# Kernel tuning notes

Hardware: AMD Instinct MI355X
Metric: run time of the kernel (lower is better)

## Reference

```python
import jax, jax.numpy as jnp
import numpy as np

B = 512
N_ENT = 100000
N_REL = 64
D = 200          # embed_dim
D1 = 10          # embed_shape (emb_dim1)
D2 = 20          # embed_dim // embed_shape (emb_dim2)
K = 3            # kernel_size
C = 32           # out_channels
FC_IN = C * (2 * D1 - K + 1) * (D2 - K + 1)  # 32*18*18 = 10368
EPS = 1e-5       # BatchNorm eps
LS = 0.1         # label_smoothing
LAM = 1e-5       # kg_l2_loss_lambda


def setup_inputs() -> dict:
    key = jax.random.key(0)
    ks = jax.random.split(key, 8)
    return dict(
        entity_w=jax.random.normal(ks[0], (N_ENT, D), jnp.float32) * 0.1,
        relation_w=jax.random.normal(ks[1], (N_REL, D), jnp.float32) * 0.1,
        conv_w=jax.random.normal(ks[2], (C, 1, K, K), jnp.float32) * 0.1,
        conv_b=jnp.zeros((C,), jnp.float32),
        fc_w=jax.random.normal(ks[3], (D, FC_IN), jnp.float32) * 0.02,
        fc_b=jnp.zeros((D,), jnp.float32),
        b=jnp.zeros((N_ENT,), jnp.float32),
        bn0_g=jnp.ones((1,), jnp.float32), bn0_b=jnp.zeros((1,), jnp.float32),
        bn1_g=jnp.ones((C,), jnp.float32), bn1_b=jnp.zeros((C,), jnp.float32),
        bn2_g=jnp.ones((D,), jnp.float32), bn2_b=jnp.zeros((D,), jnp.float32),
        h=jax.random.randint(ks[4], (B,), 0, N_ENT),
        r=jax.random.randint(ks[5], (B,), 0, N_REL),
        pos_t=jax.random.randint(ks[6], (B,), 0, N_ENT),
    )


def _bn(x, g, b, axes, shape):
    # training-mode batchnorm (batch statistics), biased variance as in torch
    m = jnp.mean(x, axes, keepdims=True)
    v = jnp.var(x, axes, keepdims=True)
    return (x - m) * jax.lax.rsqrt(v + EPS) * g.reshape(shape) + b.reshape(shape)


def _l2_mean(x):
    # torch: mean(sum(x**2, dim=1) / 2)
    return jnp.mean(jnp.sum(x * x, axis=1) / 2.0)


def reference(entity_w, relation_w, conv_w, conv_b, fc_w, fc_b, b,
              bn0_g, bn0_b, bn1_g, bn1_b, bn2_g, bn2_b, h, r, pos_t):
    h_e = entity_w[h].reshape(B, 1, D1, D2)
    r_e = relation_w[r].reshape(B, 1, D1, D2)
    x = jnp.concatenate([h_e, r_e], axis=2)           # [B,1,2*D1,D2]
    x = _bn(x, bn0_g, bn0_b, (0, 2, 3), (1, 1, 1, 1))
    x = jax.lax.conv_general_dilated(
        x, conv_w, (1, 1), 'VALID',
        dimension_numbers=('NCHW', 'OIHW', 'NCHW')) + conv_b.reshape(1, C, 1, 1)
    x = _bn(x, bn1_g, bn1_b, (0, 2, 3), (1, C, 1, 1))
    x = jax.nn.relu(x).reshape(B, -1)                 # [B, FC_IN]
    x = x @ fc_w.T + fc_b                             # [B, D]
    x = _bn(x, bn2_g, bn2_b, (0,), (1, D))
    x = jax.nn.leaky_relu(x)                          # slope 0.01 = torch default
    scores = x @ entity_w.T + b                       # [B, N_ENT]
    # BCEWithLogits with smoothed label y = (1-LS)*onehot(pos_t) + 1/N_ENT,
    # loss = mean(softplus(s) - s*y); one-hot never materialized.
    sp_sum = jnp.sum(jax.nn.softplus(scores))
    xy_sum = jnp.sum(scores) / N_ENT + (1.0 - LS) * jnp.sum(
        scores[jnp.arange(B), pos_t])
    kg_loss = (sp_sum - xy_sum) / (B * N_ENT)
    l2 = _l2_mean(h_e) + _l2_mean(r_e) + _l2_mean(conv_w) + _l2_mean(fc_w)
    return kg_loss + LAM * l2
```

## Files before the change

### kernel.cpp

```cpp
#include <hip/hip_runtime.h>
#include <math.h>

#define NB_B 512
#define NE 100000
#define DD 200
#define CC 32
#define FCIN 10368
#define HW 324
#define BNEPS 1e-5f
#define KP 224
#define NTILE 1563

typedef __attribute__((ext_vector_type(8))) short short8;
typedef __attribute__((ext_vector_type(4))) float floatx4;


static __device__ __forceinline__ float blk_reduce(float v, volatile float* sbuf) {
  for (int o = 32; o > 0; o >>= 1) v += __shfl_down(v, o, 64);
  int lane = threadIdx.x & 63, wid = threadIdx.x >> 6;
  if (lane == 0) sbuf[wid] = v;
  __syncthreads();
  float r = 0.f;
  int nw = (blockDim.x + 63) >> 6;
  if ((int)threadIdx.x < nw) r = sbuf[threadIdx.x];
  if (threadIdx.x < 64) {
    for (int o = 32; o > 0; o >>= 1) r += __shfl_down(r, o, 64);
  }
  __syncthreads();
  return r;
}

static __device__ __forceinline__ unsigned short f32_to_bf16(float f) {
  unsigned int u = __float_as_uint(f);
  u += 0x7fffu + ((u >> 16) & 1u);
  return (unsigned short)(u >> 16);
}
static __device__ __forceinline__ float bf16_to_f32(unsigned short b) {
  return __uint_as_float(((unsigned int)b) << 16);
}

__global__ void k_gather(const float* __restrict__ ent, const float* __restrict__ rel,
                         const int* __restrict__ h, const int* __restrict__ r,
                         float* __restrict__ x0, double* dacc) {
  int b = blockIdx.x;
  int hi = h[b], ri = r[b];
  float s = 0.f, sq = 0.f;
  for (int i = threadIdx.x; i < 400; i += blockDim.x) {
    float v = (i < 200) ? ent[(long)hi * DD + i] : rel[(long)ri * DD + (i - 200)];
    x0[b * 400 + i] = v;
    s += v; sq += v * v;
  }
  __shared__ float sbuf[8];
  float ts = blk_reduce(s, sbuf);
  float tq = blk_reduce(sq, sbuf);
  if (threadIdx.x == 0) {
    atomicAdd(&dacc[0], (double)ts);
    atomicAdd(&dacc[1], (double)tq);
  }
}

__global__ __launch_bounds__(256) void k_cvt(const float* __restrict__ ent,
                                             unsigned short* __restrict__ entb,
                                             const float* __restrict__ fcw,
                                             unsigned short* __restrict__ fcwb,
                                             double* dacc) {
  if (blockIdx.x < 21875) {
    int i4 = blockIdx.x * 256 + threadIdx.x;
    int row = i4 / 56;
    int c4 = (i4 - row * 56) * 4;
    ushort4 o;
    if (c4 < 200) {
      const float4 v = *(const float4*)&ent[(long)row * DD + c4];
      o.x = f32_to_bf16(v.x); o.y = f32_to_bf16(v.y);
      o.z = f32_to_bf16(v.z); o.w = f32_to_bf16(v.w);
    } else {
      o.x = 0; o.y = 0; o.z = 0; o.w = 0;
    }
    *(ushort4*)&entb[(long)row * KP + c4] = o;
  } else {
    int g = (blockIdx.x - 21875) * 256 + threadIdx.x;
    float sq = 0.f;
    if (g < 259200) {
      const float4* s = (const float4*)(fcw + (long)g * 8);
      float4 u = s[0], v = s[1];
      sq = u.x*u.x + u.y*u.y + u.z*u.z + u.w*u.w
         + v.x*v.x + v.y*v.y + v.z*v.z + v.w*v.w;
      ushort4 o0, o1;
      o0.x = f32_to_bf16(u.x); o0.y = f32_to_bf16(u.y);
      o0.z = f32_to_bf16(u.z); o0.w = f32_to_bf16(u.w);
      o1.x = f32_to_bf16(v.x); o1.y = f32_to_bf16(v.y);
      o1.z = f32_to_bf16(v.z); o1.w = f32_to_bf16(v.w);
      ushort4* d = (ushort4*)(fcwb + (long)g * 8);
      d[0] = o0; d[1] = o1;
    }
    __shared__ float sbuf[8];
    float tq = blk_reduce(sq, sbuf);
    if (threadIdx.x == 0) atomicAdd(&dacc[67], (double)tq);
  }
}

__global__ __launch_bounds__(256) void k_conv(const float* __restrict__ x0,
                       const float* __restrict__ convw, const float* __restrict__ convb,
                       const float* __restrict__ g0, const float* __restrict__ b0,
                       unsigned short* __restrict__ yb, double* dacc) {
  __shared__ float xs[400], wsm[288], cbs[32], ssum[32], ssq[32];
  __shared__ float a0s, s0s;
  int b = blockIdx.x, t = threadIdx.x;
  for (int i = t; i < 400; i += 256) xs[i] = x0[b * 400 + i];
  for (int i = t; i < 288; i += 256) wsm[i] = convw[i];
  if (t < 32) cbs[t] = convb[t];
  if (t == 0) {
    double m = dacc[0] / 204800.0;
    double v = dacc[1] / 204800.0 - m * m;
    float a = g0[0] * rsqrtf((float)v + BNEPS);
    a0s = a; s0s = b0[0] - (float)m * a;
  }
  __syncthreads();
  float a0 = a0s, s0 = s0s;
  for (int i = t; i < 400; i += 256) xs[i] = a0 * xs[i] + s0;
  __syncthreads();
  int c = t >> 3, sub = t & 7;
  const float* w = &wsm[c * 9];
  float cb = cbs[c];
  float s = 0.f, sq = 0.f;
  for (int e = sub; e < HW; e += 8) {
    int oh = e / 18, ow = e - oh * 18;
    const float* xp = &xs[oh * 20 + ow];
    float acc = cb
       + xp[0] * w[0] + xp[1] * w[1] + xp[2] * w[2]
       + xp[20] * w[3] + xp[21] * w[4] + xp[22] * w[5]
       + xp[40] * w[6] + xp[41] * w[7] + xp[42] * w[8];
    yb[(long)b * FCIN + c * HW + e] = f32_to_bf16(acc);
    s += acc; sq += acc * acc;
  }
  s += __shfl_xor(s, 1, 64); sq += __shfl_xor(sq, 1, 64);
  s += __shfl_xor(s, 2, 64); sq += __shfl_xor(sq, 2, 64);
  s += __shfl_xor(s, 4, 64); sq += __shfl_xor(sq, 4, 64);
  if (sub == 0) { ssum[c] = s; ssq[c] = sq; }
  __syncthreads();
  if (t < 32) {
    atomicAdd(&dacc[2 + t], (double)ssum[t]);
    atomicAdd(&dacc[34 + t], (double)ssq[t]);
  }
}

__global__ void k_stats1(const float* __restrict__ g1, const float* __restrict__ b1,
                         const float* __restrict__ convw,
                         float* __restrict__ a1, float* __restrict__ sh1, double* dacc) {
  int t = threadIdx.x;
  if (t < 32) {
    double cnt = 512.0 * 324.0;
    double m = dacc[2 + t] / cnt, v = dacc[34 + t] / cnt - m * m;
    float a = g1[t] * rsqrtf((float)v + BNEPS);
    a1[t] = a; sh1[t] = b1[t] - (float)m * a;
  }
  float sq = 0.f;
  for (int i = t; i < 288; i += 64) { float w = convw[i]; sq += w * w; }
  for (int o = 32; o > 0; o >>= 1) sq += __shfl_down(sq, o, 64);
  if (t == 0) dacc[66] = (double)sq;
}

__global__ __launch_bounds__(256) void k_prep(unsigned short* __restrict__ yb,
                                              const float* __restrict__ a1,
                                              const float* __restrict__ sh1) {
  __shared__ float a1s[32], sh1s[32];
  int t = threadIdx.x;
  if (t < 32) { a1s[t] = a1[t]; sh1s[t] = sh1[t]; }
  __syncthreads();
  int g = blockIdx.x * 256 + t;
  int row = g / 1296;
  int c8 = (g - row * 1296) * 8;
  unsigned short* p = yb + (long)row * FCIN + c8;
  ushort4 v0 = ((ushort4*)p)[0], v1 = ((ushort4*)p)[1];
  unsigned short e[8] = {v0.x, v0.y, v0.z, v0.w, v1.x, v1.y, v1.z, v1.w};
#pragma unroll
  for (int j = 0; j < 8; j++) {
    int c = (c8 + j) / HW;
    float f = a1s[c] * bf16_to_f32(e[j]) + sh1s[c];
    e[j] = f32_to_bf16(fmaxf(f, 0.f));
  }
  v0.x = e[0]; v0.y = e[1]; v0.z = e[2]; v0.w = e[3];
  v1.x = e[4]; v1.y = e[5]; v1.z = e[6]; v1.w = e[7];
  ((ushort4*)p)[0] = v0; ((ushort4*)p)[1] = v1;
}

__global__ __launch_bounds__(64) void k_fc_mfma(const unsigned short* __restrict__ yb,
                                                const unsigned short* __restrict__ fcwb,
                                                float* __restrict__ Cfc) {
  int wid = blockIdx.x;
  int ks = wid >> 5, rem = wid & 31;
  int mt = rem >> 2, nt = rem & 3;
  int lane = threadIdx.x;
  int quad = lane >> 4, lr = lane & 15;
  int m0 = mt * 64, n0 = nt * 64;
  int kbeg = ks * 192;

  const unsigned short* arow[4];
  const unsigned short* brow[4];
#pragma unroll
  for (int mi = 0; mi < 4; mi++)
    arow[mi] = yb + (long)(m0 + mi * 16 + lr) * FCIN + quad * 8 + kbeg;
#pragma unroll
  for (int ni = 0; ni < 4; ni++) {
    int d = n0 + ni * 16 + lr;
    if (d > DD - 1) d = DD - 1;
    brow[ni] = fcwb + (long)d * FCIN + quad * 8 + kbeg;
  }

  floatx4 acc[4][4];
#pragma unroll
  for (int i = 0; i < 4; i++)
#pragma unroll
    for (int j = 0; j < 4; j++) acc[i][j] = (floatx4){0.f, 0.f, 0.f, 0.f};

  short8 acur[4], bcur[4], anxt[4], bnxt[4];
#pragma unroll
  for (int mi = 0; mi < 4; mi++) acur[mi] = *(const short8*)(arow[mi]);
#pragma unroll
  for (int ni = 0; ni < 4; ni++) bcur[ni] = *(const short8*)(brow[ni]);

#pragma unroll
  for (int c = 0; c < 6; c++) {
    if (c < 5) {
#pragma unroll
      for (int mi = 0; mi < 4; mi++) anxt[mi] = *(const short8*)(arow[mi] + (c + 1) * 32);
#pragma unroll
      for (int ni = 0; ni < 4; ni++) bnxt[ni] = *(const short8*)(brow[ni] + (c + 1) * 32);
    }
#pragma unroll
    for (int ni = 0; ni < 4; ni++)
#pragma unroll
      for (int mi = 0; mi < 4; mi++)
        acc[mi][ni] = __builtin_amdgcn_mfma_f32_16x16x32_bf16(acur[mi], bcur[ni], acc[mi][ni], 0, 0, 0);
#pragma unroll
    for (int mi = 0; mi < 4; mi++) acur[mi] = anxt[mi];
#pragma unroll
    for (int ni = 0; ni < 4; ni++) bcur[ni] = bnxt[ni];
  }

#pragma unroll
  for (int ni = 0; ni < 4; ni++) {
    int d = n0 + ni * 16 + lr;
    if (d < DD) {
#pragma unroll
      for (int mi = 0; mi < 4; mi++) {
        int mbase = m0 + mi * 16 + quad * 4;
#pragma unroll
        for (int rg = 0; rg < 4; rg++)
          atomicAdd(&Cfc[(mbase + rg) * DD + d], acc[mi][ni][rg]);
      }
    }
  }
}

__global__ void k_bn2stats(const float* __restrict__ Cfc, const float* __restrict__ fcb,
                           const float* __restrict__ g2, const float* __restrict__ b2,
                           float* __restrict__ a2, float* __restrict__ b2c) {
  int d = blockIdx.x, lane = threadIdx.x;
  float s = 0.f, sq = 0.f;
  for (int b = lane; b < NB_B; b += 64) {
    float v = Cfc[b * DD + d] + fcb[d];
    s += v; sq += v * v;
  }
  for (int o = 32; o > 0; o >>= 1) { s += __shfl_down(s, o, 64); sq += __shfl_down(sq, o, 64); }
  if (lane == 0) {
    float m = s / 512.f, v = sq / 512.f - m * m;
    float a = g2[d] * rsqrtf(v + BNEPS);
    a2[d] = a; b2c[d] = b2[d] - m * a;
  }
}

__global__ __launch_bounds__(256) void k_xfinal(const float* __restrict__ Cfc,
                         const float* __restrict__ fcb,
                         const float* __restrict__ a2, const float* __restrict__ b2c,
                         const float* __restrict__ ent, const float* __restrict__ bias,
                         const int* __restrict__ pos,
                         float* __restrict__ xf, unsigned short* __restrict__ xfb,
                         double* dacc) {
  __shared__ float xs[224];
  __shared__ float sbuf[8];
  int b = blockIdx.x, t = threadIdx.x;
  if (t < KP) {
    float xv = 0.f;
    if (t < DD) {
      float v = Cfc[b * DD + t] + fcb[t];
      xv = a2[t] * v + b2c[t];
      xv = xv >= 0.f ? xv : 0.01f * xv;
      xf[b * DD + t] = xv;
    }
    xfb[b * KP + t] = f32_to_bf16(xv);
    xs[t] = xv;
  }
  __syncthreads();
  int e = pos[b];
  float s = (t < DD) ? xs[t] * ent[(long)e * DD + t] : 0.f;
  float ts = blk_reduce(s, sbuf);
  if (t == 0) atomicAdd(&dacc[70], (double)(ts + bias[e]));
}

__global__ __launch_bounds__(512, 2) void k_scores2(
    const unsigned short* __restrict__ entb,
    const unsigned short* __restrict__ xfb,
    const float* __restrict__ bias, double* dacc) {
  __shared__ float sbuf[8];
  int t = threadIdx.x;
  int wv = t >> 6, lane = t & 63;
  int quad = lane >> 4, lr = lane & 15;

  short8 af[4][7];
#pragma unroll
  for (int mi = 0; mi < 4; mi++) {
    const unsigned short* ap = xfb + (size_t)(wv * 64 + mi * 16 + lr) * KP + quad * 8;
#pragma unroll
    for (int kc = 0; kc < 7; kc++) af[mi][kc] = *(const short8*)(ap + kc * 32);
  }

  float sp = 0.f, ss = 0.f;
  for (int tile = blockIdx.x; tile < NTILE; tile += gridDim.x) {
    int e0 = tile * 64;
    const unsigned short* bp[4];
    int eidx[4];
#pragma unroll
    for (int ni = 0; ni < 4; ni++) {
      int e = e0 + ni * 16 + lr;
      eidx[ni] = e;
      if (e > NE - 1) e = NE - 1;
      bp[ni] = entb + (size_t)e * KP + quad * 8;
    }
    floatx4 acc[4][4];
#pragma unroll
    for (int i = 0; i < 4; i++)
#pragma unroll
      for (int j = 0; j < 4; j++) acc[i][j] = (floatx4){0.f, 0.f, 0.f, 0.f};

    short8 bcur[4], bnxt[4];
#pragma unroll
    for (int ni = 0; ni < 4; ni++) bcur[ni] = *(const short8*)(bp[ni]);
#pragma unroll
    for (int kc = 0; kc < 7; kc++) {
      if (kc < 6) {
#pragma unroll
        for (int ni = 0; ni < 4; ni++) bnxt[ni] = *(const short8*)(bp[ni] + (kc + 1) * 32);
      }
#pragma unroll
      for (int ni = 0; ni < 4; ni++)
#pragma unroll
        for (int mi = 0; mi < 4; mi++)
          acc[mi][ni] = __builtin_amdgcn_mfma_f32_16x16x32_bf16(af[mi][kc], bcur[ni], acc[mi][ni], 0, 0, 0);
#pragma unroll
      for (int ni = 0; ni < 4; ni++) bcur[ni] = bnxt[ni];
    }
#pragma unroll
    for (int ni = 0; ni < 4; ni++) {
      if (eidx[ni] < NE) {
        float be = bias[eidx[ni]];
#pragma unroll
        for (int mi = 0; mi < 4; mi++) {
#pragma unroll
          for (int rg = 0; rg < 4; rg++) {
            float s = acc[mi][ni][rg] + be;
            sp += fmaxf(s, 0.f) + __logf(1.f + __expf(-fabsf(s)));
            ss += s;
          }
        }
      }
    }
  }
  float tsp = blk_reduce(sp, sbuf);
  float tss = blk_reduce(ss, sbuf);
  if (t == 0) {
    atomicAdd(&dacc[68], (double)tsp);
    atomicAdd(&dacc[69], (double)tss);
  }
}

__global__ void k_final(const double* dacc, float* out) {
  double SP = dacc[68], S2 = dacc[69], S3 = dacc[70];
  double xy = S2 / (double)NE + 0.9 * S3;
  double kg = (SP - xy) / ((double)NB_B * (double)NE);
  double l2 = dacc[1] / 204800.0 + dacc[66] / 576.0 + dacc[67] / 400.0;
  out[0] = (float)(kg + 1e-5 * l2);
}

extern "C" void kernel_launch(void* const* d_in, const int* in_sizes, int n_in,
                              void* d_out, int out_size, void* d_ws, size_t ws_size,
                              hipStream_t stream) {
  const float* ent   = (const float*)d_in[0];
  const float* rel   = (const float*)d_in[1];
  const float* convw = (const float*)d_in[2];
  const float* convb = (const float*)d_in[3];
  const float* fcw   = (const float*)d_in[4];
  const float* fcb   = (const float*)d_in[5];
  const float* bias  = (const float*)d_in[6];
  const float* g0    = (const float*)d_in[7];
  const float* b0    = (const float*)d_in[8];
  const float* g1    = (const float*)d_in[9];
  const float* b1    = (const float*)d_in[10];
  const float* g2    = (const float*)d_in[11];
  const float* b2    = (const float*)d_in[12];
  const int*   h     = (const int*)d_in[13];
  const int*   r     = (const int*)d_in[14];
  const int*   pos   = (const int*)d_in[15];

  char* ws = (char*)d_ws;
  double* dacc = (double*)(ws + 0);
  float* a1  = (float*)(ws + 16384);
  float* sh1 = (float*)(ws + 16384 + 128);
  float* a2  = (float*)(ws + 16384 + 256);
  float* b2c = (float*)(ws + 16384 + 1056);
  float* x0  = (float*)(ws + 32768);
  float* Cfc = (float*)(ws + 851968);
  float* xf  = (float*)(ws + 1261568);
  unsigned short* yb   = (unsigned short*)(ws + 1671168);
  unsigned short* fcwb = (unsigned short*)(ws + 12288000);
  unsigned short* xfb  = (unsigned short*)(ws + 16435200);
  unsigned short* entb = (unsigned short*)(ws + 16664576);

  hipMemsetAsync(dacc, 0, 8192, stream);
  hipMemsetAsync(Cfc, 0, 409600, stream);

  k_cvt<<<22888, 256, 0, stream>>>(ent, entb, fcw, fcwb, dacc);
  k_gather<<<512, 256, 0, stream>>>(ent, rel, h, r, x0, dacc);
  k_conv<<<512, 256, 0, stream>>>(x0, convw, convb, g0, b0, yb, dacc);
  k_stats1<<<1, 64, 0, stream>>>(g1, b1, convw, a1, sh1, dacc);
  k_prep<<<2592, 256, 0, stream>>>(yb, a1, sh1);
  k_fc_mfma<<<1728, 64, 0, stream>>>(yb, fcwb, Cfc);
  k_bn2stats<<<200, 64, 0, stream>>>(Cfc, fcb, g2, b2, a2, b2c);
  k_xfinal<<<512, 256, 0, stream>>>(Cfc, fcb, a2, b2c, ent, bias, pos, xf, xfb, dacc);
  k_scores2<<<256, 512, 0, stream>>>(entb, xfb, bias, dacc);
  k_final<<<1, 1, 0, stream>>>(dacc, (float*)d_out);
}
```

Baseline: 328.9 us.

## Fuse gather into convert, drop stats kernel, rework FC and scores grids

Folds the gather into the bf16 convert kernel and widens its per-thread work to 8 elements. The BN1 stats computation moves into k_prep and the conv-weight L2 into k_final, which removes a launch. The FC GEMM becomes 32 blocks of 4 waves that split K and reduce through shared memory, replacing atomics and the Cfc memset. The scores kernel is regridded to 391x4 blocks of 256 threads, each wave handling 32 rows, with double-buffered B loads. Together this cuts launches and atomic traffic, but the FC stage now runs on only 32 blocks, which risks low GPU occupancy.

```diff
diff --git a/kernel.cpp b/kernel.cpp
--- a/kernel.cpp
+++ b/kernel.cpp
@@ -11,6 +11,10 @@
 #define KP 224
 #define NTILE 1563
 
+#define ENT_BLKS 10938
+#define FCW_BLKS 1013
+#define GATH_OFF (ENT_BLKS + FCW_BLKS)
+
 typedef __attribute__((ext_vector_type(8))) short short8;
 typedef __attribute__((ext_vector_type(4))) float floatx4;
 
@@ -39,46 +43,37 @@
   return __uint_as_float(((unsigned int)b) << 16);
 }
 
-__global__ void k_gather(const float* __restrict__ ent, const float* __restrict__ rel,
-                         const int* __restrict__ h, const int* __restrict__ r,
-                         float* __restrict__ x0, double* dacc) {
-  int b = blockIdx.x;
-  int hi = h[b], ri = r[b];
-  float s = 0.f, sq = 0.f;
-  for (int i = threadIdx.x; i < 400; i += blockDim.x) {
-    float v = (i < 200) ? ent[(long)hi * DD + i] : rel[(long)ri * DD + (i - 200)];
-    x0[b * 400 + i] = v;
-    s += v; sq += v * v;
-  }
-  __shared__ float sbuf[8];
-  float ts = blk_reduce(s, sbuf);
-  float tq = blk_reduce(sq, sbuf);
-  if (threadIdx.x == 0) {
-    atomicAdd(&dacc[0], (double)ts);
-    atomicAdd(&dacc[1], (double)tq);
-  }
-}
-
 __global__ __launch_bounds__(256) void k_cvt(const float* __restrict__ ent,
                                              unsigned short* __restrict__ entb,
                                              const float* __restrict__ fcw,
                                              unsigned short* __restrict__ fcwb,
+                                             const float* __restrict__ rel,
+                                             const int* __restrict__ h,
+                                             const int* __restrict__ r,
+                                             float* __restrict__ x0,
                                              double* dacc) {
-  if (blockIdx.x < 21875) {
-    int i4 = blockIdx.x * 256 + threadIdx.x;
-    int row = i4 / 56;
-    int c4 = (i4 - row * 56) * 4;
-    ushort4 o;
-    if (c4 < 200) {
-      const float4 v = *(const float4*)&ent[(long)row * DD + c4];
-      o.x = f32_to_bf16(v.x); o.y = f32_to_bf16(v.y);
-      o.z = f32_to_bf16(v.z); o.w = f32_to_bf16(v.w);
-    } else {
-      o.x = 0; o.y = 0; o.z = 0; o.w = 0;
-    }
-    *(ushort4*)&entb[(long)row * KP + c4] = o;
-  } else {
-    int g = (blockIdx.x - 21875) * 256 + threadIdx.x;
+  if (blockIdx.x < ENT_BLKS) {
+    int g = blockIdx.x * 256 + threadIdx.x;
+    if (g < 2800000) {
+      int row = g / 28;
+      int c8 = (g - row * 28) * 8;
+      ushort4 o0, o1;
+      if (c8 < 200) {
+        const float4* s = (const float4*)(ent + (long)row * DD + c8);
+        float4 u = s[0], v = s[1];
+        o0.x = f32_to_bf16(u.x); o0.y = f32_to_bf16(u.y);
+        o0.z = f32_to_bf16(u.z); o0.w = f32_to_bf16(u.w);
+        o1.x = f32_to_bf16(v.x); o1.y = f32_to_bf16(v.y);
+        o1.z = f32_to_bf16(v.z); o1.w = f32_to_bf16(v.w);
+      } else {
+        o0.x = o0.y = o0.z = o0.w = 0;
+        o1.x = o1.y = o1.z = o1.w = 0;
+      }
+      ushort4* d = (ushort4*)(entb + (long)row * KP + c8);
+      d[0] = o0; d[1] = o1;
+    }
+  } else if (blockIdx.x < GATH_OFF) {
+    int g = (blockIdx.x - ENT_BLKS) * 256 + threadIdx.x;
     float sq = 0.f;
     if (g < 259200) {
       const float4* s = (const float4*)(fcw + (long)g * 8);
@@ -96,6 +91,22 @@
     __shared__ float sbuf[8];
     float tq = blk_reduce(sq, sbuf);
     if (threadIdx.x == 0) atomicAdd(&dacc[67], (double)tq);
+  } else {
+    int b = blockIdx.x - GATH_OFF;
+    int hi = h[b], ri = r[b];
+    float s = 0.f, sq = 0.f;
+    for (int i = threadIdx.x; i < 400; i += 256) {
+      float v = (i < 200) ? ent[(long)hi * DD + i] : rel[(long)ri * DD + (i - 200)];
+      x0[b * 400 + i] = v;
+      s += v; sq += v * v;
+    }
+    __shared__ float sbuf[8];
+    float ts = blk_reduce(s, sbuf);
+    float tq = blk_reduce(sq, sbuf);
+    if (threadIdx.x == 0) {
+      atomicAdd(&dacc[0], (double)ts);
+      atomicAdd(&dacc[1], (double)tq);
+    }
   }
 }
 
@@ -144,28 +155,18 @@
   }
 }
 
-__global__ void k_stats1(const float* __restrict__ g1, const float* __restrict__ b1,
-                         const float* __restrict__ convw,
-                         float* __restrict__ a1, float* __restrict__ sh1, double* dacc) {
+__global__ __launch_bounds__(256) void k_prep(unsigned short* __restrict__ yb,
+                                              const float* __restrict__ g1,
+                                              const float* __restrict__ b1,
+                                              const double* __restrict__ dacc) {
+  __shared__ float a1s[32], sh1s[32];
   int t = threadIdx.x;
   if (t < 32) {
     double cnt = 512.0 * 324.0;
     double m = dacc[2 + t] / cnt, v = dacc[34 + t] / cnt - m * m;
     float a = g1[t] * rsqrtf((float)v + BNEPS);
-    a1[t] = a; sh1[t] = b1[t] - (float)m * a;
-  }
-  float sq = 0.f;
-  for (int i = t; i < 288; i += 64) { float w = convw[i]; sq += w * w; }
-  for (int o = 32; o > 0; o >>= 1) sq += __shfl_down(sq, o, 64);
-  if (t == 0) dacc[66] = (double)sq;
-}
-
-__global__ __launch_bounds__(256) void k_prep(unsigned short* __restrict__ yb,
-                                              const float* __restrict__ a1,
-                                              const float* __restrict__ sh1) {
-  __shared__ float a1s[32], sh1s[32];
-  int t = threadIdx.x;
-  if (t < 32) { a1s[t] = a1[t]; sh1s[t] = sh1[t]; }
+    a1s[t] = a; sh1s[t] = b1[t] - (float)m * a;
+  }
   __syncthreads();
   int g = blockIdx.x * 256 + t;
   int row = g / 1296;
@@ -184,27 +185,27 @@
   ((ushort4*)p)[0] = v0; ((ushort4*)p)[1] = v1;
 }
 
-__global__ __launch_bounds__(64) void k_fc_mfma(const unsigned short* __restrict__ yb,
+__global__ __launch_bounds__(256, 2) void k_fc2(const unsigned short* __restrict__ yb,
                                                 const unsigned short* __restrict__ fcwb,
                                                 float* __restrict__ Cfc) {
-  int wid = blockIdx.x;
-  int ks = wid >> 5, rem = wid & 31;
-  int mt = rem >> 2, nt = rem & 3;
-  int lane = threadIdx.x;
+  __shared__ float red[4][64][64];
+  int bid = blockIdx.x;
+  int mt = bid >> 2, nt = bid & 3;
+  int m0 = mt * 64, n0 = nt * 64;
+  int t = threadIdx.x, wv = t >> 6, lane = t & 63;
   int quad = lane >> 4, lr = lane & 15;
-  int m0 = mt * 64, n0 = nt * 64;
-  int kbeg = ks * 192;
+  long kbeg = (long)wv * 2592;
 
   const unsigned short* arow[4];
   const unsigned short* brow[4];
 #pragma unroll
   for (int mi = 0; mi < 4; mi++)
-    arow[mi] = yb + (long)(m0 + mi * 16 + lr) * FCIN + quad * 8 + kbeg;
+    arow[mi] = yb + (long)(m0 + mi * 16 + lr) * FCIN + kbeg + quad * 8;
 #pragma unroll
   for (int ni = 0; ni < 4; ni++) {
     int d = n0 + ni * 16 + lr;
     if (d > DD - 1) d = DD - 1;
-    brow[ni] = fcwb + (long)d * FCIN + quad * 8 + kbeg;
+    brow[ni] = fcwb + (long)d * FCIN + kbeg + quad * 8;
   }
 
   floatx4 acc[4][4];
@@ -213,42 +214,48 @@
 #pragma unroll
     for (int j = 0; j < 4; j++) acc[i][j] = (floatx4){0.f, 0.f, 0.f, 0.f};
 
-  short8 acur[4], bcur[4], anxt[4], bnxt[4];
-#pragma unroll
-  for (int mi = 0; mi < 4; mi++) acur[mi] = *(const short8*)(arow[mi]);
-#pragma unroll
-  for (int ni = 0; ni < 4; ni++) bcur[ni] = *(const short8*)(brow[ni]);
-
-#pragma unroll
-  for (int c = 0; c < 6; c++) {
-    if (c < 5) {
-#pragma unroll
-      for (int mi = 0; mi < 4; mi++) anxt[mi] = *(const short8*)(arow[mi] + (c + 1) * 32);
-#pragma unroll
-      for (int ni = 0; ni < 4; ni++) bnxt[ni] = *(const short8*)(brow[ni] + (c + 1) * 32);
-    }
+  short8 sA[3][4], sB[3][4];
+#pragma unroll
+  for (int c = 0; c < 3; c++) {
+#pragma unroll
+    for (int mi = 0; mi < 4; mi++) sA[c][mi] = *(const short8*)(arow[mi] + c * 32);
+#pragma unroll
+    for (int ni = 0; ni < 4; ni++) sB[c][ni] = *(const short8*)(brow[ni] + c * 32);
+  }
+  for (int c3 = 0; c3 < 27; c3++) {
+    int cc = c3 * 3;
+#pragma unroll
+    for (int j = 0; j < 3; j++) {
+#pragma unroll
+      for (int ni = 0; ni < 4; ni++)
+#pragma unroll
+        for (int mi = 0; mi < 4; mi++)
+          acc[mi][ni] = __builtin_amdgcn_mfma_f32_16x16x32_bf16(sA[j][mi], sB[j][ni], acc[mi][ni], 0, 0, 0);
+      int nxt = cc + j + 3;
+      if (nxt < 81) {
+#pragma unroll
+        for (int mi = 0; mi < 4; mi++) sA[j][mi] = *(const short8*)(arow[mi] + nxt * 32);
+#pragma unroll
+        for (int ni = 0; ni < 4; ni++) sB[j][ni] = *(const short8*)(brow[ni] + nxt * 32);
+      }
+    }
+  }
+
+#pragma unroll
+  for (int mi = 0; mi < 4; mi++)
 #pragma unroll
     for (int ni = 0; ni < 4; ni++)
 #pragma unroll
-      for (int mi = 0; mi < 4; mi++)
-        acc[mi][ni] = __builtin_amdgcn_mfma_f32_16x16x32_bf16(acur[mi], bcur[ni], acc[mi][ni], 0, 0, 0);
-#pragma unroll
-    for (int mi = 0; mi < 4; mi++) acur[mi] = anxt[mi];
-#pragma unroll
-    for (int ni = 0; ni < 4; ni++) bcur[ni] = bnxt[ni];
-  }
-
-#pragma unroll
-  for (int ni = 0; ni < 4; ni++) {
-    int d = n0 + ni * 16 + lr;
-    if (d < DD) {
-#pragma unroll
-      for (int mi = 0; mi < 4; mi++) {
-        int mbase = m0 + mi * 16 + quad * 4;
-#pragma unroll
-        for (int rg = 0; rg < 4; rg++)
-          atomicAdd(&Cfc[(mbase + rg) * DD + d], acc[mi][ni][rg]);
-      }
+      for (int rg = 0; rg < 4; rg++)
+        red[wv][mi * 16 + quad * 4 + rg][ni * 16 + lr] = acc[mi][ni][rg];
+  __syncthreads();
+#pragma unroll
+  for (int i = 0; i < 16; i++) {
+    int o = t + 256 * i;
+    int row = o >> 6, col = o & 63;
+    if (n0 + col < DD) {
+      float v = red[0][row][col] + red[1][row][col] + red[2][row][col] + red[3][row][col];
+      Cfc[(m0 + row) * DD + n0 + col] = v;
     }
   }
 }
@@ -298,7 +305,7 @@
   if (t == 0) atomicAdd(&dacc[70], (double)(ts + bias[e]));
 }
 
-__global__ __launch_bounds__(512, 2) void k_scores2(
+__global__ __launch_bounds__(256, 3) void k_scores2(
     const unsigned short* __restrict__ entb,
     const unsigned short* __restrict__ xfb,
     const float* __restrict__ bias, double* dacc) {
@@ -306,17 +313,18 @@
   int t = threadIdx.x;
   int wv = t >> 6, lane = t & 63;
   int quad = lane >> 4, lr = lane & 15;
-
-  short8 af[4][7];
-#pragma unroll
-  for (int mi = 0; mi < 4; mi++) {
-    const unsigned short* ap = xfb + (size_t)(wv * 64 + mi * 16 + lr) * KP + quad * 8;
+  int rowbase = blockIdx.y * 128 + wv * 32;
+
+  short8 af[2][7];
+#pragma unroll
+  for (int mi = 0; mi < 2; mi++) {
+    const unsigned short* ap = xfb + (size_t)(rowbase + mi * 16 + lr) * KP + quad * 8;
 #pragma unroll
     for (int kc = 0; kc < 7; kc++) af[mi][kc] = *(const short8*)(ap + kc * 32);
   }
 
   float sp = 0.f, ss = 0.f;
-  for (int tile = blockIdx.x; tile < NTILE; tile += gridDim.x) {
+  for (int tile = blockIdx.x; tile < NTILE; tile += 391) {
     int e0 = tile * 64;
     const unsigned short* bp[4];
     int eidx[4];
@@ -327,35 +335,36 @@
       if (e > NE - 1) e = NE - 1;
       bp[ni] = entb + (size_t)e * KP + quad * 8;
     }
-    floatx4 acc[4][4];
-#pragma unroll
-    for (int i = 0; i < 4; i++)
+    floatx4 acc[2][4];
+#pragma unroll
+    for (int i = 0; i < 2; i++)
 #pragma unroll
       for (int j = 0; j < 4; j++) acc[i][j] = (floatx4){0.f, 0.f, 0.f, 0.f};
 
-    short8 bcur[4], bnxt[4];
-#pragma unroll
-    for (int ni = 0; ni < 4; ni++) bcur[ni] = *(const short8*)(bp[ni]);
+    short8 bs[2][4];
+#pragma unroll
+    for (int ni = 0; ni < 4; ni++) bs[0][ni] = *(const short8*)(bp[ni]);
+#pragma unroll
+    for (int ni = 0; ni < 4; ni++) bs[1][ni] = *(const short8*)(bp[ni] + 32);
 #pragma unroll
     for (int kc = 0; kc < 7; kc++) {
-      if (kc < 6) {
-#pragma unroll
-        for (int ni = 0; ni < 4; ni++) bnxt[ni] = *(const short8*)(bp[ni] + (kc + 1) * 32);
+      int s = kc & 1;
+#pragma unroll
+      for (int ni = 0; ni < 4; ni++)
+#pragma unroll
+        for (int mi = 0; mi < 2; mi++)
+          acc[mi][ni] = __builtin_amdgcn_mfma_f32_16x16x32_bf16(af[mi][kc], bs[s][ni], acc[mi][ni], 0, 0, 0);
+      if (kc + 2 < 7) {
+#pragma unroll
+        for (int ni = 0; ni < 4; ni++) bs[s][ni] = *(const short8*)(bp[ni] + (kc + 2) * 32);
       }
-#pragma unroll
-      for (int ni = 0; ni < 4; ni++)
-#pragma unroll
-        for (int mi = 0; mi < 4; mi++)
-          acc[mi][ni] = __builtin_amdgcn_mfma_f32_16x16x32_bf16(af[mi][kc], bcur[ni], acc[mi][ni], 0, 0, 0);
-#pragma unroll
-      for (int ni = 0; ni < 4; ni++) bcur[ni] = bnxt[ni];
     }
 #pragma unroll
     for (int ni = 0; ni < 4; ni++) {
       if (eidx[ni] < NE) {
         float be = bias[eidx[ni]];
 #pragma unroll
-        for (int mi = 0; mi < 4; mi++) {
+        for (int mi = 0; mi < 2; mi++) {
 #pragma unroll
           for (int rg = 0; rg < 4; rg++) {
             float s = acc[mi][ni][rg] + be;
@@ -374,12 +383,18 @@
   }
 }
 
-__global__ void k_final(const double* dacc, float* out) {
-  double SP = dacc[68], S2 = dacc[69], S3 = dacc[70];
-  double xy = S2 / (double)NE + 0.9 * S3;
-  double kg = (SP - xy) / ((double)NB_B * (double)NE);
-  double l2 = dacc[1] / 204800.0 + dacc[66] / 576.0 + dacc[67] / 400.0;
-  out[0] = (float)(kg + 1e-5 * l2);
+__global__ void k_final(const float* __restrict__ convw, const double* dacc, float* out) {
+  int t = threadIdx.x;
+  float sq = 0.f;
+  for (int i = t; i < 288; i += 64) { float w = convw[i]; sq += w * w; }
+  for (int o = 32; o > 0; o >>= 1) sq += __shfl_down(sq, o, 64);
+  if (t == 0) {
+    double SP = dacc[68], S2 = dacc[69], S3 = dacc[70];
+    double xy = S2 / (double)NE + 0.9 * S3;
+    double kg = (SP - xy) / ((double)NB_B * (double)NE);
+    double l2 = dacc[1] / 204800.0 + (double)sq / 576.0 + dacc[67] / 400.0;
+    out[0] = (float)(kg + 1e-5 * l2);
+  }
 }
 
 extern "C" void kernel_launch(void* const* d_in, const int* in_sizes, int n_in,
@@ -404,8 +419,6 @@
 
   char* ws = (char*)d_ws;
   double* dacc = (double*)(ws + 0);
-  float* a1  = (float*)(ws + 16384);
-  float* sh1 = (float*)(ws + 16384 + 128);
   float* a2  = (float*)(ws + 16384 + 256);
   float* b2c = (float*)(ws + 16384 + 1056);
   float* x0  = (float*)(ws + 32768);
@@ -417,16 +430,13 @@
   unsigned short* entb = (unsigned short*)(ws + 16664576);
 
   hipMemsetAsync(dacc, 0, 8192, stream);
-  hipMemsetAsync(Cfc, 0, 409600, stream);
-
-  k_cvt<<<22888, 256, 0, stream>>>(ent, entb, fcw, fcwb, dacc);
-  k_gather<<<512, 256, 0, stream>>>(ent, rel, h, r, x0, dacc);
+
+  k_cvt<<<GATH_OFF + 512, 256, 0, stream>>>(ent, entb, fcw, fcwb, rel, h, r, x0, dacc);
   k_conv<<<512, 256, 0, stream>>>(x0, convw, convb, g0, b0, yb, dacc);
-  k_stats1<<<1, 64, 0, stream>>>(g1, b1, convw, a1, sh1, dacc);
-  k_prep<<<2592, 256, 0, stream>>>(yb, a1, sh1);
-  k_fc_mfma<<<1728, 64, 0, stream>>>(yb, fcwb, Cfc);
+  k_prep<<<2592, 256, 0, stream>>>(yb, g1, b1, dacc);
+  k_fc2<<<32, 256, 0, stream>>>(yb, fcwb, Cfc);
   k_bn2stats<<<200, 64, 0, stream>>>(Cfc, fcb, g2, b2, a2, b2c);
   k_xfinal<<<512, 256, 0, stream>>>(Cfc, fcb, a2, b2c, ent, bias, pos, xf, xfb, dacc);
-  k_scores2<<<256, 512, 0, stream>>>(entb, xfb, bias, dacc);
-  k_final<<<1, 1, 0, stream>>>(dacc, (float*)d_out);
-}
+  k_scores2<<<dim3(391, 4), 256, 0, stream>>>(entb, xfb, bias, dacc);
+  k_final<<<1, 64, 0, stream>>>(convw, dacc, (float*)d_out);
+}
```

Result: slower. 384.8 us (+17.0%).
